# Optimization experiments

Measured on AMD Instinct MI355X. Metric: run time of the kernel, lower is better.

The kernel has to match this reference:

```python
import jax, jax.numpy as jnp
import numpy as np

B, C, H, W = 16, 256, 32, 32
AD, SC, R = 16, 32, 4


def _conv1x1(x, w, b):
    # x: [B,Cin,H,W], w: [Cout,Cin], b: [Cout]
    return jnp.einsum('oc,bchw->bohw', w, x) + b[None, :, None, None]


def setup_inputs() -> dict:
    key = jax.random.key(0)
    ks = jax.random.split(key, 12)
    p = lambda k, shape: (jax.random.normal(k, shape, dtype=jnp.float32) * 0.02)
    return {
        'x': jax.random.normal(ks[0], (B, C, H, W), dtype=jnp.float32),
        'fc1_w': p(ks[1], (C // R, C)), 'fc1_b': jnp.zeros((C // R,), jnp.float32),
        'fc2_w': p(ks[2], (C, C // R)), 'fc2_b': jnp.zeros((C,), jnp.float32),
        'qkv_w': p(ks[3], (AD * 2 + SC, SC)), 'qkv_b': jnp.zeros((AD * 2 + SC,), jnp.float32),
        'proj_w': p(ks[4], (SC, SC)), 'proj_b': jnp.zeros((SC,), jnp.float32),
        'ffn1_w': p(ks[5], (4 * C, C)), 'ffn1_b': jnp.zeros((4 * C,), jnp.float32),
        'ffn2_w': p(ks[6], (C, 4 * C)), 'ffn2_b': jnp.zeros((C,), jnp.float32),
    }


def reference(x, fc1_w, fc1_b, fc2_w, fc2_b, qkv_w, qkv_b, proj_w, proj_b,
              ffn1_w, ffn1_b, ffn2_w, ffn2_b):
    # --- DynamicChannelSelect: SE gate then channel split ---
    s = x.mean(axis=(2, 3), keepdims=True)                       # [B,C,1,1]
    s = jax.nn.relu(_conv1x1(s, fc1_w, fc1_b))
    s = jax.nn.sigmoid(_conv1x1(s, fc2_w, fc2_b))
    xg = x * s
    attn_part, non_attn_part = xg[:, :SC], xg[:, SC:]

    # --- SHSA: single-head self-attention on SC channels ---
    qkv = _conv1x1(attn_part, qkv_w, qkv_b)                      # [B,2*AD+SC,H,W]
    q = qkv[:, :AD].reshape(B, AD, H * W)
    k = qkv[:, AD:2 * AD].reshape(B, AD, H * W)
    v = qkv[:, 2 * AD:].reshape(B, SC, H * W)
    scale = AD ** -0.5
    attn = jax.nn.softmax(jnp.einsum('bcn,bcm->bnm', q, k) * scale, axis=-1)  # [B,N,N]
    out = jnp.einsum('bcm,bnm->bcn', v, attn).reshape(B, SC, H, W)
    attn_out = _conv1x1(out, proj_w, proj_b)

    # --- concat + 1x1-conv FFN ---
    y = jnp.concatenate([attn_out, non_attn_part], axis=1)       # [B,C,H,W]
    h = jax.nn.relu(_conv1x1(y, ffn1_w, ffn1_b))                 # [B,4C,H,W]
    return _conv1x1(h, ffn2_w, ffn2_b)                           # [B,C,H,W]
```

## Files before the change

### kernel.cpp

```cpp
#include <hip/hip_runtime.h>
#include <cstdint>
#include <cstddef>

#define BB 16
#define CC 256
#define NP 1024

typedef __attribute__((ext_vector_type(8))) short bf16x8;
typedef __attribute__((ext_vector_type(4))) float f32x4;
typedef unsigned short u16;

__device__ __forceinline__ u16 f2bf(float f) {
    union { float f; uint32_t u; } v; v.f = f;
    uint32_t u = v.u;
    return (u16)((u + 0x7FFFu + ((u >> 16) & 1u)) >> 16);
}

__global__ __launch_bounds__(256)
void se_mean_kernel(const float* __restrict__ x, float* __restrict__ s_mean) {
    int bc = blockIdx.x;
    const float* p = x + (size_t)bc * NP;
    int t = threadIdx.x;
    float4 v = *(const float4*)(p + t * 4);
    float s = (v.x + v.y) + (v.z + v.w);
#pragma unroll
    for (int off = 32; off; off >>= 1) s += __shfl_down(s, off, 64);
    __shared__ float red[4];
    if ((t & 63) == 0) red[t >> 6] = s;
    __syncthreads();
    if (t == 0) s_mean[bc] = (red[0] + red[1] + red[2] + red[3]) * (1.0f / NP);
}

__global__ __launch_bounds__(256)
void se_mlp_kernel(const float* __restrict__ s_mean,
                   const float* __restrict__ fc1_w, const float* __restrict__ fc1_b,
                   const float* __restrict__ fc2_w, const float* __restrict__ fc2_b,
                   float* __restrict__ sig) {
    int b = blockIdx.x;
    __shared__ float sm[CC];
    __shared__ float h1[64];
    int t = threadIdx.x;
    sm[t] = s_mean[b * CC + t];
    __syncthreads();
    if (t < 64) {
        float a = fc1_b[t];
        for (int c = 0; c < CC; ++c) a += fc1_w[t * CC + c] * sm[c];
        h1[t] = fmaxf(a, 0.f);
    }
    __syncthreads();
    float a = fc2_b[t];
#pragma unroll 8
    for (int c = 0; c < 64; ++c) a += fc2_w[t * 64 + c] * h1[c];
    sig[b * CC + t] = 1.f / (1.f + __expf(-a));
}

__global__ __launch_bounds__(256)
void scale_transpose_qkv_kernel(const float* __restrict__ x, const float* __restrict__ sig,
                                const float* __restrict__ qW, const float* __restrict__ qB,
                                u16* __restrict__ ygt, u16* __restrict__ Qt,
                                u16* __restrict__ Kt, u16* __restrict__ Vb) {
    int nt = blockIdx.x, ct = blockIdx.y, b = blockIdx.z;
    __shared__ float tile[64][65];
    __shared__ float ws[64 * 32];
    __shared__ float bs[64];
    __shared__ float vtile[32][64];
    int t = threadIdx.x;
    const float* Xb = x + ((size_t)b * CC + ct * 64) * NP + nt * 64;
    if (ct == 0) {
        for (int e = t; e < 2048; e += 256) ws[e] = qW[e];
        if (t < 64) bs[t] = qB[t];
    }
#pragma unroll
    for (int p = 0; p < 4; ++p) {
        int e = t + p * 256;
        int c = e >> 4, n4 = (e & 15) * 4;
        float4 v = *(const float4*)&Xb[(size_t)c * NP + n4];
        float sc = sig[b * CC + ct * 64 + c];
        v.x *= sc; v.y *= sc; v.z *= sc; v.w *= sc;
        tile[c][n4] = v.x; tile[c][n4 + 1] = v.y; tile[c][n4 + 2] = v.z; tile[c][n4 + 3] = v.w;
    }
    __syncthreads();
    u16* Yb = ygt + ((size_t)b * NP + nt * 64) * CC + ct * 64;
#pragma unroll
    for (int p = 0; p < 4; ++p) {
        int e = t + p * 256;
        int n = e >> 4, c4 = (e & 15) * 4;
        if (ct * 64 + c4 >= 32) {
            ushort4 o;
            o.x = f2bf(tile[c4][n]);     o.y = f2bf(tile[c4 + 1][n]);
            o.z = f2bf(tile[c4 + 2][n]); o.w = f2bf(tile[c4 + 3][n]);
            *(ushort4*)&Yb[(size_t)n * CC + c4] = o;
        }
    }
    if (ct == 0) {
        int nn = t & 63, g = t >> 6;
        int n = nt * 64 + nn;
        float acc[16];
#pragma unroll
        for (int oc = 0; oc < 16; ++oc) {
            int o = g * 16 + oc;
            float a = bs[o];
#pragma unroll
            for (int c = 0; c < 32; ++c) a += ws[o * 32 + c] * tile[c][nn];
            acc[oc] = a;
        }
        if (g == 0) {
            u16* qr = Qt + ((size_t)b * NP + n) * 32;
            ushort4 z4; z4.x = 0; z4.y = 0; z4.z = 0; z4.w = 0;
#pragma unroll
            for (int j = 0; j < 16; j += 4) {
                ushort4 o4;
                o4.x = f2bf(acc[j] * 0.25f);     o4.y = f2bf(acc[j + 1] * 0.25f);
                o4.z = f2bf(acc[j + 2] * 0.25f); o4.w = f2bf(acc[j + 3] * 0.25f);
                *(ushort4*)&qr[j] = o4;
            }
            *(ushort4*)&qr[16] = z4; *(ushort4*)&qr[20] = z4;
            *(ushort4*)&qr[24] = z4; *(ushort4*)&qr[28] = z4;
        } else if (g == 1) {
            u16* kr = Kt + ((size_t)b * NP + n) * 32;
            ushort4 z4; z4.x = 0; z4.y = 0; z4.z = 0; z4.w = 0;
#pragma unroll
            for (int j = 0; j < 16; j += 4) {
                ushort4 k4;
                k4.x = f2bf(acc[j]);     k4.y = f2bf(acc[j + 1]);
                k4.z = f2bf(acc[j + 2]); k4.w = f2bf(acc[j + 3]);
                *(ushort4*)&kr[j] = k4;
            }
            *(ushort4*)&kr[16] = z4; *(ushort4*)&kr[20] = z4;
            *(ushort4*)&kr[24] = z4; *(ushort4*)&kr[28] = z4;
        } else {
#pragma unroll
            for (int oc = 0; oc < 16; ++oc) vtile[(g - 2) * 16 + oc][nn] = acc[oc];
        }
        __syncthreads();
        for (int e = t; e < 2048; e += 256) {
            int c = e >> 6, nn2 = e & 63;
            Vb[(size_t)b * 32 * NP + (size_t)c * NP + nt * 64 + nn2] = f2bf(vtile[c][nn2]);
        }
    }
}

__global__ __launch_bounds__(512)
void attn_mfma_kernel(const u16* __restrict__ Qt, const u16* __restrict__ Kt,
                      const u16* __restrict__ Vb,
                      const float* __restrict__ proj_w, const float* __restrict__ proj_b,
                      u16* __restrict__ ygt) {
    int b = blockIdx.x >> 4;
    int n0 = (blockIdx.x & 15) * 64;
    __shared__ __align__(16) u16 P_lds[8][16][40];
    __shared__ float al_lds[8][16];
    __shared__ float sm_lds[8][16];
    __shared__ float sl_lds[8][16];
    __shared__ float O_lds[8][16][33];
    __shared__ float pw_s[32][32];
    __shared__ float pb_s[32];
    int t = threadIdx.x;
    int w = t >> 6, lane = t & 63;
    int q = lane >> 4, idx = lane & 15;
    int rg = w & 3, kh = w >> 2;

    for (int e = t; e < 1024; e += 512) pw_s[e >> 5][e & 31] = proj_w[e];
    if (t < 32) pb_s[t] = proj_b[t];
    __syncthreads();

    const u16* Qb = Qt + (size_t)b * NP * 32;
    const u16* Kb = Kt + (size_t)b * NP * 32;
    const u16* Vp = Vb + (size_t)b * 32 * NP;

    int nrow = n0 + rg * 16 + idx;
    bf16x8 aq = *(const bf16x8*)&Qb[(size_t)nrow * 32 + q * 8];

    f32x4 O0 = {0.f, 0.f, 0.f, 0.f}, O1 = {0.f, 0.f, 0.f, 0.f};
    float m_run[4] = {-1e30f, -1e30f, -1e30f, -1e30f};
    float l_run[4] = {0.f, 0.f, 0.f, 0.f};

    int mbase = kh * 512;
    for (int m0 = mbase; m0 < mbase + 512; m0 += 32) {
        bf16x8 bk0 = *(const bf16x8*)&Kb[(size_t)(m0 + idx) * 32 + q * 8];
        bf16x8 bk1 = *(const bf16x8*)&Kb[(size_t)(m0 + 16 + idx) * 32 + q * 8];
        bf16x8 va0 = *(const bf16x8*)&Vp[(size_t)idx * NP + m0 + q * 8];
        bf16x8 va1 = *(const bf16x8*)&Vp[(size_t)(16 + idx) * NP + m0 + q * 8];
        f32x4 z = {0.f, 0.f, 0.f, 0.f};
        f32x4 S0 = __builtin_amdgcn_mfma_f32_16x16x32_bf16(aq, bk0, z, 0, 0, 0);
        f32x4 S1 = __builtin_amdgcn_mfma_f32_16x16x32_bf16(aq, bk1, z, 0, 0, 0);
        float mx[4], p0[4], p1[4], alpha[4];
#pragma unroll
        for (int r = 0; r < 4; ++r) mx[r] = fmaxf(S0[r], S1[r]);
#pragma unroll
        for (int off = 1; off < 16; off <<= 1)
#pragma unroll
            for (int r = 0; r < 4; ++r) mx[r] = fmaxf(mx[r], __shfl_xor(mx[r], off, 64));
#pragma unroll
        for (int r = 0; r < 4; ++r) {
            float nm = fmaxf(m_run[r], mx[r]);
            alpha[r] = __expf(m_run[r] - nm);
            m_run[r] = nm;
            p0[r] = __expf(S0[r] - nm);
            p1[r] = __expf(S1[r] - nm);
        }
#pragma unroll
        for (int r = 0; r < 4; ++r) {
            float s = p0[r] + p1[r];
#pragma unroll
            for (int off = 1; off < 16; off <<= 1) s += __shfl_xor(s, off, 64);
            l_run[r] = l_run[r] * alpha[r] + s;
        }
#pragma unroll
        for (int r = 0; r < 4; ++r) {
            P_lds[w][q * 4 + r][idx]      = f2bf(p0[r]);
            P_lds[w][q * 4 + r][idx + 16] = f2bf(p1[r]);
        }
        if (idx == 0) {
#pragma unroll
            for (int r = 0; r < 4; ++r) al_lds[w][q * 4 + r] = alpha[r];
        }
        float an = al_lds[w][idx];
#pragma unroll
        for (int r = 0; r < 4; ++r) { O0[r] *= an; O1[r] *= an; }
        bf16x8 pf = *(const bf16x8*)&P_lds[w][idx][q * 8];
        O0 = __builtin_amdgcn_mfma_f32_16x16x32_bf16(va0, pf, O0, 0, 0, 0);
        O1 = __builtin_amdgcn_mfma_f32_16x16x32_bf16(va1, pf, O1, 0, 0, 0);
    }
    if (idx == 0) {
#pragma unroll
        for (int r = 0; r < 4; ++r) {
            sm_lds[w][q * 4 + r] = m_run[r];
            sl_lds[w][q * 4 + r] = l_run[r];
        }
    }
#pragma unroll
    for (int r = 0; r < 4; ++r) {
        O_lds[w][idx][q * 4 + r]      = O0[r];
        O_lds[w][idx][q * 4 + r + 16] = O1[r];
    }
    __syncthreads();
    if (w < 4) {
        float ma = sm_lds[w][idx], mb = sm_lds[w + 4][idx];
        float la = sl_lds[w][idx], lb = sl_lds[w + 4][idx];
        float gm = fmaxf(ma, mb);
        float ea = __expf(ma - gm), eb = __expf(mb - gm);
        float linv = 1.f / (la * ea + lb * eb);
#pragma unroll
        for (int r = 0; r < 4; ++r) {
            int c0 = q * 4 + r;
            O_lds[w][idx][c0]      = (O_lds[w][idx][c0] * ea + O_lds[w + 4][idx][c0] * eb) * linv;
            O_lds[w][idx][c0 + 16] = (O_lds[w][idx][c0 + 16] * ea + O_lds[w + 4][idx][c0 + 16] * eb) * linv;
        }
        float o0[4], o1[4];
#pragma unroll
        for (int r = 0; r < 4; ++r) { o0[r] = pb_s[q * 4 + r]; o1[r] = pb_s[q * 4 + r + 16]; }
#pragma unroll
        for (int c = 0; c < 32; ++c) {
            float xv = O_lds[w][idx][c];
#pragma unroll
            for (int r = 0; r < 4; ++r) {
                o0[r] += pw_s[q * 4 + r][c] * xv;
                o1[r] += pw_s[q * 4 + r + 16][c] * xv;
            }
        }
        u16* yrow = ygt + ((size_t)b * NP + n0 + w * 16 + idx) * CC;
        ushort4 w0, w1;
        w0.x = f2bf(o0[0]); w0.y = f2bf(o0[1]); w0.z = f2bf(o0[2]); w0.w = f2bf(o0[3]);
        w1.x = f2bf(o1[0]); w1.y = f2bf(o1[1]); w1.z = f2bf(o1[2]); w1.w = f2bf(o1[3]);
        *(ushort4*)&yrow[q * 4] = w0;
        *(ushort4*)&yrow[q * 4 + 16] = w1;
    }
}

__global__ __launch_bounds__(256)
void convert_w_kernel(const float* __restrict__ w1, u16* __restrict__ d1,
                      const float* __restrict__ w2, u16* __restrict__ d2) {
    int blk = blockIdx.x;
    const float* src = (blk < 256) ? w1 : w2;
    u16* dst = (blk < 256) ? d1 : d2;
    int i = ((blk & 255) * 256 + threadIdx.x) * 4;
    float4 v = *(const float4*)(src + i);
    ushort4 o;
    o.x = f2bf(v.x); o.y = f2bf(v.y); o.z = f2bf(v.z); o.w = f2bf(v.w);
    *(ushort4*)(dst + i) = o;
}

template <int K, bool RELU, bool TRANS_OUT>
__global__ __launch_bounds__(256)
void mfma_gemm_kernel(const u16* __restrict__ A, const u16* __restrict__ Bt,
                      const float* __restrict__ bias, void* __restrict__ Yv, int M) {
    __shared__ __align__(16) u16 As[2][128][64];
    __shared__ __align__(16) u16 Bs[2][128][64];
    constexpr int NIT = K / 64;
    int mt = blockIdx.x, nt = blockIdx.y;
    const u16* Ab = A + (size_t)mt * 128 * K;
    const u16* Bb = Bt + (size_t)nt * 128 * K;
    int t = threadIdx.x;
    int w = t >> 6, lane = t & 63;
    int q = lane >> 4, idx = lane & 15;
    int wr = (w >> 1) * 64, wc = (w & 1) * 64;
    int srow = lane >> 3;
    int gch = (lane & 7) ^ srow;

    f32x4 acc[4][4];
#pragma unroll
    for (int i = 0; i < 4; ++i)
#pragma unroll
        for (int j = 0; j < 4; ++j) { f32x4 z = {0.f, 0.f, 0.f, 0.f}; acc[i][j] = z; }

#define ISSUE_LOADS(buf, k0)                                                              \
    {                                                                                     \
        _Pragma("unroll")                                                                 \
        for (int p = 0; p < 4; ++p) {                                                     \
            int r = w * 32 + p * 8 + srow;                                                \
            __builtin_amdgcn_global_load_lds(                                             \
                (const __attribute__((address_space(1))) void*)(Ab + (size_t)r * K + (k0) + gch * 8), \
                (__attribute__((address_space(3))) void*)(&As[buf][w * 32 + p * 8][0]),   \
                16, 0, 0);                                                                \
        }                                                                                 \
        _Pragma("unroll")                                                                 \
        for (int p = 0; p < 4; ++p) {                                                     \
            int r = w * 32 + p * 8 + srow;                                                \
            __builtin_amdgcn_global_load_lds(                                             \
                (const __attribute__((address_space(1))) void*)(Bb + (size_t)r * K + (k0) + gch * 8), \
                (__attribute__((address_space(3))) void*)(&Bs[buf][w * 32 + p * 8][0]),   \
                16, 0, 0);                                                                \
        }                                                                                 \
    }

    ISSUE_LOADS(0, 0)
    for (int ki = 0; ki < NIT; ++ki) {
        int cur = ki & 1;
        __syncthreads();
        if (ki + 1 < NIT) ISSUE_LOADS(cur ^ 1, (ki + 1) * 64)
#pragma unroll
        for (int h = 0; h < 2; ++h) {
            bf16x8 af[4], bfr[4];
#pragma unroll
            for (int i = 0; i < 4; ++i)
                af[i] = *(const bf16x8*)&As[cur][wr + i * 16 + idx][(((q + 4 * h) ^ (idx & 7)) * 8)];
#pragma unroll
            for (int j = 0; j < 4; ++j)
                bfr[j] = *(const bf16x8*)&Bs[cur][wc + j * 16 + idx][(((q + 4 * h) ^ (idx & 7)) * 8)];
#pragma unroll
            for (int i = 0; i < 4; ++i)
#pragma unroll
                for (int j = 0; j < 4; ++j)
                    acc[i][j] = __builtin_amdgcn_mfma_f32_16x16x32_bf16(af[i], bfr[j], acc[i][j], 0, 0, 0);
        }
    }
#undef ISSUE_LOADS

    if (TRANS_OUT) {
        u16* Y = (u16*)Yv;
#pragma unroll
        for (int i = 0; i < 4; ++i) {
            int m0 = mt * 128 + wr + i * 16 + q * 4;
            float b0 = bias[m0], b1 = bias[m0 + 1], b2 = bias[m0 + 2], b3 = bias[m0 + 3];
#pragma unroll
            for (int j = 0; j < 4; ++j) {
                int n = nt * 128 + wc + j * 16 + idx;
                f32x4 v = acc[i][j];
                float r0 = v.x + b0, r1 = v.y + b1, r2 = v.z + b2, r3 = v.w + b3;
                if (RELU) {
                    r0 = fmaxf(r0, 0.f); r1 = fmaxf(r1, 0.f);
                    r2 = fmaxf(r2, 0.f); r3 = fmaxf(r3, 0.f);
                }
                ushort4 o;
                o.x = f2bf(r0); o.y = f2bf(r1); o.z = f2bf(r2); o.w = f2bf(r3);
                *(ushort4*)&Y[(size_t)n * (size_t)M + m0] = o;
            }
        }
    } else {
        float* Y = (float*)Yv;
#pragma unroll
        for (int i = 0; i < 4; ++i) {
            int m0 = mt * 128 + wr + i * 16 + q * 4;
            float b0 = bias[m0], b1 = bias[m0 + 1], b2 = bias[m0 + 2], b3 = bias[m0 + 3];
#pragma unroll
            for (int j = 0; j < 4; ++j) {
                int ng = nt * 128 + wc + j * 16 + idx;
                int bb = ng >> 10, nn = ng & 1023;
                f32x4 v = acc[i][j];
                float* p = Y + ((size_t)bb * M + m0) * NP + nn;
                p[0]      = v.x + b0;
                p[NP]     = v.y + b1;
                p[2 * NP] = v.z + b2;
                p[3 * NP] = v.w + b3;
            }
        }
    }
}

extern "C" void kernel_launch(void* const* d_in, const int* in_sizes, int n_in,
                              void* d_out, int out_size, void* d_ws, size_t ws_size,
                              hipStream_t stream) {
    const float* x      = (const float*)d_in[0];
    const float* fc1_w  = (const float*)d_in[1];
    const float* fc1_b  = (const float*)d_in[2];
    const float* fc2_w  = (const float*)d_in[3];
    const float* fc2_b  = (const float*)d_in[4];
    const float* qkv_w  = (const float*)d_in[5];
    const float* qkv_b  = (const float*)d_in[6];
    const float* proj_w = (const float*)d_in[7];
    const float* proj_b = (const float*)d_in[8];
    const float* ffn1_w = (const float*)d_in[9];
    const float* ffn1_b = (const float*)d_in[10];
    const float* ffn2_w = (const float*)d_in[11];
    const float* ffn2_b = (const float*)d_in[12];
    float* out = (float*)d_out;

    u16* w1b = (u16*)d_ws;
    u16* w2b = w1b + 262144;
    u16* ygt = w2b + 262144;
    u16* ht  = ygt + (size_t)BB * NP * CC;
    float* sig    = (float*)ht;
    float* s_mean = sig + BB * CC;
    u16* Qt = (u16*)(s_mean + BB * CC);
    u16* Kt = Qt + (size_t)BB * NP * 32;
    u16* Vb = Kt + (size_t)BB * NP * 32;

    se_mean_kernel<<<BB * CC, 256, 0, stream>>>(x, s_mean);
    convert_w_kernel<<<512, 256, 0, stream>>>(ffn1_w, w1b, ffn2_w, w2b);
    se_mlp_kernel<<<BB, 256, 0, stream>>>(s_mean, fc1_w, fc1_b, fc2_w, fc2_b, sig);
    scale_transpose_qkv_kernel<<<dim3(16, 4, BB), 256, 0, stream>>>(
        x, sig, qkv_w, qkv_b, ygt, Qt, Kt, Vb);
    attn_mfma_kernel<<<BB * 16, 512, 0, stream>>>(Qt, Kt, Vb, proj_w, proj_b, ygt);

    mfma_gemm_kernel<256, true, true><<<dim3(8, 128), 256, 0, stream>>>(
        w1b, ygt, ffn1_b, (void*)ht, 1024);
    mfma_gemm_kernel<1024, false, false><<<dim3(2, 128), 256, 0, stream>>>(
        w2b, ht, ffn2_b, (void*)out, 256);
}
```

Before: 181.7 us.

## Split attention into more blocks, add N64 FFN2 GEMM tile, fuse SE mean and weight conversion

The attention kernel now handles 16 query rows per block with 4 waves, each covering a quarter of the keys, instead of 64 rows with 8 waves. That gives four times as many blocks, and the partial softmax states are merged 4-way in LDS. The second FFN GEMM gets a dedicated kernel with a 128x64 tile, doubling its grid from 256 to 512 blocks so more CUs are busy. The SE mean kernel and the weight bf16 conversion are merged into one launch. The cost is more redundant K/V and proj-weight loads across blocks, and a serial 4-way merge done by a single wave.

Result: no change. 180.1 us (-0.9%).

```diff
diff --git a/kernel.cpp b/kernel.cpp
--- a/kernel.cpp
+++ b/kernel.cpp
@@ -17,18 +17,31 @@
 }
 
 __global__ __launch_bounds__(256)
-void se_mean_kernel(const float* __restrict__ x, float* __restrict__ s_mean) {
-    int bc = blockIdx.x;
-    const float* p = x + (size_t)bc * NP;
-    int t = threadIdx.x;
-    float4 v = *(const float4*)(p + t * 4);
-    float s = (v.x + v.y) + (v.z + v.w);
-#pragma unroll
-    for (int off = 32; off; off >>= 1) s += __shfl_down(s, off, 64);
-    __shared__ float red[4];
-    if ((t & 63) == 0) red[t >> 6] = s;
-    __syncthreads();
-    if (t == 0) s_mean[bc] = (red[0] + red[1] + red[2] + red[3]) * (1.0f / NP);
+void se_mean_conv_kernel(const float* __restrict__ x, float* __restrict__ s_mean,
+                         const float* __restrict__ w1, u16* __restrict__ d1,
+                         const float* __restrict__ w2, u16* __restrict__ d2) {
+    int blk = blockIdx.x;
+    int t = threadIdx.x;
+    if (blk < BB * CC) {
+        const float* p = x + (size_t)blk * NP;
+        float4 v = *(const float4*)(p + t * 4);
+        float s = (v.x + v.y) + (v.z + v.w);
+#pragma unroll
+        for (int off = 32; off; off >>= 1) s += __shfl_down(s, off, 64);
+        __shared__ float red[4];
+        if ((t & 63) == 0) red[t >> 6] = s;
+        __syncthreads();
+        if (t == 0) s_mean[blk] = (red[0] + red[1] + red[2] + red[3]) * (1.0f / NP);
+    } else {
+        int blk2 = blk - BB * CC;
+        const float* src = (blk2 < 256) ? w1 : w2;
+        u16* dst = (blk2 < 256) ? d1 : d2;
+        int i = ((blk2 & 255) * 256 + t) * 4;
+        float4 v = *(const float4*)(src + i);
+        ushort4 o;
+        o.x = f2bf(v.x); o.y = f2bf(v.y); o.z = f2bf(v.z); o.w = f2bf(v.w);
+        *(ushort4*)(dst + i) = o;
+    }
 }
 
 __global__ __launch_bounds__(256)
@@ -140,26 +153,25 @@
     }
 }
 
-__global__ __launch_bounds__(512)
+__global__ __launch_bounds__(256)
 void attn_mfma_kernel(const u16* __restrict__ Qt, const u16* __restrict__ Kt,
                       const u16* __restrict__ Vb,
                       const float* __restrict__ proj_w, const float* __restrict__ proj_b,
                       u16* __restrict__ ygt) {
-    int b = blockIdx.x >> 4;
-    int n0 = (blockIdx.x & 15) * 64;
-    __shared__ __align__(16) u16 P_lds[8][16][40];
-    __shared__ float al_lds[8][16];
-    __shared__ float sm_lds[8][16];
-    __shared__ float sl_lds[8][16];
-    __shared__ float O_lds[8][16][33];
+    int b = blockIdx.x >> 6;
+    int n0 = (blockIdx.x & 63) * 16;
+    __shared__ __align__(16) u16 P_lds[4][16][40];
+    __shared__ float al_lds[4][16];
+    __shared__ float sm_lds[4][16];
+    __shared__ float sl_lds[4][16];
+    __shared__ float O_lds[4][16][33];
     __shared__ float pw_s[32][32];
     __shared__ float pb_s[32];
     int t = threadIdx.x;
     int w = t >> 6, lane = t & 63;
     int q = lane >> 4, idx = lane & 15;
-    int rg = w & 3, kh = w >> 2;
-
-    for (int e = t; e < 1024; e += 512) pw_s[e >> 5][e & 31] = proj_w[e];
+
+    for (int e = t; e < 1024; e += 256) pw_s[e >> 5][e & 31] = proj_w[e];
     if (t < 32) pb_s[t] = proj_b[t];
     __syncthreads();
 
@@ -167,15 +179,15 @@
     const u16* Kb = Kt + (size_t)b * NP * 32;
     const u16* Vp = Vb + (size_t)b * 32 * NP;
 
-    int nrow = n0 + rg * 16 + idx;
+    int nrow = n0 + idx;
     bf16x8 aq = *(const bf16x8*)&Qb[(size_t)nrow * 32 + q * 8];
 
     f32x4 O0 = {0.f, 0.f, 0.f, 0.f}, O1 = {0.f, 0.f, 0.f, 0.f};
     float m_run[4] = {-1e30f, -1e30f, -1e30f, -1e30f};
     float l_run[4] = {0.f, 0.f, 0.f, 0.f};
 
-    int mbase = kh * 512;
-    for (int m0 = mbase; m0 < mbase + 512; m0 += 32) {
+    int mbase = w * 256;
+    for (int m0 = mbase; m0 < mbase + 256; m0 += 32) {
         bf16x8 bk0 = *(const bf16x8*)&Kb[(size_t)(m0 + idx) * 32 + q * 8];
         bf16x8 bk1 = *(const bf16x8*)&Kb[(size_t)(m0 + 16 + idx) * 32 + q * 8];
         bf16x8 va0 = *(const bf16x8*)&Vp[(size_t)idx * NP + m0 + q * 8];
@@ -234,31 +246,35 @@
         O_lds[w][idx][q * 4 + r + 16] = O1[r];
     }
     __syncthreads();
-    if (w < 4) {
-        float ma = sm_lds[w][idx], mb = sm_lds[w + 4][idx];
-        float la = sl_lds[w][idx], lb = sl_lds[w + 4][idx];
-        float gm = fmaxf(ma, mb);
-        float ea = __expf(ma - gm), eb = __expf(mb - gm);
-        float linv = 1.f / (la * ea + lb * eb);
+    if (w == 0) {
+        float m0_ = sm_lds[0][idx], m1 = sm_lds[1][idx], m2 = sm_lds[2][idx], m3 = sm_lds[3][idx];
+        float gm = fmaxf(fmaxf(m0_, m1), fmaxf(m2, m3));
+        float e0 = __expf(m0_ - gm), e1 = __expf(m1 - gm);
+        float e2 = __expf(m2 - gm), e3 = __expf(m3 - gm);
+        float linv = 1.f / (sl_lds[0][idx] * e0 + sl_lds[1][idx] * e1 +
+                            sl_lds[2][idx] * e2 + sl_lds[3][idx] * e3);
 #pragma unroll
         for (int r = 0; r < 4; ++r) {
             int c0 = q * 4 + r;
-            O_lds[w][idx][c0]      = (O_lds[w][idx][c0] * ea + O_lds[w + 4][idx][c0] * eb) * linv;
-            O_lds[w][idx][c0 + 16] = (O_lds[w][idx][c0 + 16] * ea + O_lds[w + 4][idx][c0 + 16] * eb) * linv;
+            O_lds[0][idx][c0] = (O_lds[0][idx][c0] * e0 + O_lds[1][idx][c0] * e1 +
+                                 O_lds[2][idx][c0] * e2 + O_lds[3][idx][c0] * e3) * linv;
+            int c1 = c0 + 16;
+            O_lds[0][idx][c1] = (O_lds[0][idx][c1] * e0 + O_lds[1][idx][c1] * e1 +
+                                 O_lds[2][idx][c1] * e2 + O_lds[3][idx][c1] * e3) * linv;
         }
         float o0[4], o1[4];
 #pragma unroll
         for (int r = 0; r < 4; ++r) { o0[r] = pb_s[q * 4 + r]; o1[r] = pb_s[q * 4 + r + 16]; }
 #pragma unroll
         for (int c = 0; c < 32; ++c) {
-            float xv = O_lds[w][idx][c];
+            float xv = O_lds[0][idx][c];
 #pragma unroll
             for (int r = 0; r < 4; ++r) {
                 o0[r] += pw_s[q * 4 + r][c] * xv;
                 o1[r] += pw_s[q * 4 + r + 16][c] * xv;
             }
         }
-        u16* yrow = ygt + ((size_t)b * NP + n0 + w * 16 + idx) * CC;
+        u16* yrow = ygt + ((size_t)b * NP + n0 + idx) * CC;
         ushort4 w0, w1;
         w0.x = f2bf(o0[0]); w0.y = f2bf(o0[1]); w0.z = f2bf(o0[2]); w0.w = f2bf(o0[3]);
         w1.x = f2bf(o1[0]); w1.y = f2bf(o1[1]); w1.z = f2bf(o1[2]); w1.w = f2bf(o1[3]);
@@ -267,23 +283,10 @@
     }
 }
 
-__global__ __launch_bounds__(256)
-void convert_w_kernel(const float* __restrict__ w1, u16* __restrict__ d1,
-                      const float* __restrict__ w2, u16* __restrict__ d2) {
-    int blk = blockIdx.x;
-    const float* src = (blk < 256) ? w1 : w2;
-    u16* dst = (blk < 256) ? d1 : d2;
-    int i = ((blk & 255) * 256 + threadIdx.x) * 4;
-    float4 v = *(const float4*)(src + i);
-    ushort4 o;
-    o.x = f2bf(v.x); o.y = f2bf(v.y); o.z = f2bf(v.z); o.w = f2bf(v.w);
-    *(ushort4*)(dst + i) = o;
-}
-
-template <int K, bool RELU, bool TRANS_OUT>
+template <int K, bool RELU>
 __global__ __launch_bounds__(256)
 void mfma_gemm_kernel(const u16* __restrict__ A, const u16* __restrict__ Bt,
-                      const float* __restrict__ bias, void* __restrict__ Yv, int M) {
+                      const float* __restrict__ bias, u16* __restrict__ Y, int M) {
     __shared__ __align__(16) u16 As[2][128][64];
     __shared__ __align__(16) u16 Bs[2][128][64];
     constexpr int NIT = K / 64;
@@ -346,43 +349,106 @@
     }
 #undef ISSUE_LOADS
 
-    if (TRANS_OUT) {
-        u16* Y = (u16*)Yv;
-#pragma unroll
-        for (int i = 0; i < 4; ++i) {
-            int m0 = mt * 128 + wr + i * 16 + q * 4;
-            float b0 = bias[m0], b1 = bias[m0 + 1], b2 = bias[m0 + 2], b3 = bias[m0 + 3];
-#pragma unroll
-            for (int j = 0; j < 4; ++j) {
-                int n = nt * 128 + wc + j * 16 + idx;
-                f32x4 v = acc[i][j];
-                float r0 = v.x + b0, r1 = v.y + b1, r2 = v.z + b2, r3 = v.w + b3;
-                if (RELU) {
-                    r0 = fmaxf(r0, 0.f); r1 = fmaxf(r1, 0.f);
-                    r2 = fmaxf(r2, 0.f); r3 = fmaxf(r3, 0.f);
-                }
-                ushort4 o;
-                o.x = f2bf(r0); o.y = f2bf(r1); o.z = f2bf(r2); o.w = f2bf(r3);
-                *(ushort4*)&Y[(size_t)n * (size_t)M + m0] = o;
+#pragma unroll
+    for (int i = 0; i < 4; ++i) {
+        int m0 = mt * 128 + wr + i * 16 + q * 4;
+        float b0 = bias[m0], b1 = bias[m0 + 1], b2 = bias[m0 + 2], b3 = bias[m0 + 3];
+#pragma unroll
+        for (int j = 0; j < 4; ++j) {
+            int n = nt * 128 + wc + j * 16 + idx;
+            f32x4 v = acc[i][j];
+            float r0 = v.x + b0, r1 = v.y + b1, r2 = v.z + b2, r3 = v.w + b3;
+            if (RELU) {
+                r0 = fmaxf(r0, 0.f); r1 = fmaxf(r1, 0.f);
+                r2 = fmaxf(r2, 0.f); r3 = fmaxf(r3, 0.f);
             }
-        }
-    } else {
-        float* Y = (float*)Yv;
-#pragma unroll
-        for (int i = 0; i < 4; ++i) {
-            int m0 = mt * 128 + wr + i * 16 + q * 4;
-            float b0 = bias[m0], b1 = bias[m0 + 1], b2 = bias[m0 + 2], b3 = bias[m0 + 3];
-#pragma unroll
-            for (int j = 0; j < 4; ++j) {
-                int ng = nt * 128 + wc + j * 16 + idx;
-                int bb = ng >> 10, nn = ng & 1023;
-                f32x4 v = acc[i][j];
-                float* p = Y + ((size_t)bb * M + m0) * NP + nn;
-                p[0]      = v.x + b0;
-                p[NP]     = v.y + b1;
-                p[2 * NP] = v.z + b2;
-                p[3 * NP] = v.w + b3;
-            }
+            ushort4 o;
+            o.x = f2bf(r0); o.y = f2bf(r1); o.z = f2bf(r2); o.w = f2bf(r3);
+            *(ushort4*)&Y[(size_t)n * (size_t)M + m0] = o;
+        }
+    }
+}
+
+template <int K>
+__global__ __launch_bounds__(256)
+void mfma_gemm_n64_kernel(const u16* __restrict__ A, const u16* __restrict__ Bt,
+                          const float* __restrict__ bias, float* __restrict__ Y, int M) {
+    __shared__ __align__(16) u16 As[2][128][64];
+    __shared__ __align__(16) u16 Bs[2][64][64];
+    constexpr int NIT = K / 64;
+    int mt = blockIdx.x, nt = blockIdx.y;
+    const u16* Ab = A + (size_t)mt * 128 * K;
+    const u16* Bb = Bt + (size_t)nt * 64 * K;
+    int t = threadIdx.x;
+    int w = t >> 6, lane = t & 63;
+    int q = lane >> 4, idx = lane & 15;
+    int wr = (w >> 1) * 64, wc = (w & 1) * 32;
+    int srow = lane >> 3;
+    int gch = (lane & 7) ^ srow;
+
+    f32x4 acc[4][2];
+#pragma unroll
+    for (int i = 0; i < 4; ++i)
+#pragma unroll
+        for (int j = 0; j < 2; ++j) { f32x4 z = {0.f, 0.f, 0.f, 0.f}; acc[i][j] = z; }
+
+#define ISSUE_LOADS64(buf, k0)                                                            \
+    {                                                                                     \
+        _Pragma("unroll")                                                                 \
+        for (int p = 0; p < 4; ++p) {                                                     \
+            int r = w * 32 + p * 8 + srow;                                                \
+            __builtin_amdgcn_global_load_lds(                                             \
+                (const __attribute__((address_space(1))) void*)(Ab + (size_t)r * K + (k0) + gch * 8), \
+                (__attribute__((address_space(3))) void*)(&As[buf][w * 32 + p * 8][0]),   \
+                16, 0, 0);                                                                \
+        }                                                                                 \
+        _Pragma("unroll")                                                                 \
+        for (int p = 0; p < 2; ++p) {                                                     \
+            int r = w * 16 + p * 8 + srow;                                                \
+            __builtin_amdgcn_global_load_lds(                                             \
+                (const __attribute__((address_space(1))) void*)(Bb + (size_t)r * K + (k0) + gch * 8), \
+                (__attribute__((address_space(3))) void*)(&Bs[buf][w * 16 + p * 8][0]),   \
+                16, 0, 0);                                                                \
+        }                                                                                 \
+    }
+
+    ISSUE_LOADS64(0, 0)
+    for (int ki = 0; ki < NIT; ++ki) {
+        int cur = ki & 1;
+        __syncthreads();
+        if (ki + 1 < NIT) ISSUE_LOADS64(cur ^ 1, (ki + 1) * 64)
+#pragma unroll
+        for (int h = 0; h < 2; ++h) {
+            bf16x8 af[4], bfr[2];
+#pragma unroll
+            for (int i = 0; i < 4; ++i)
+                af[i] = *(const bf16x8*)&As[cur][wr + i * 16 + idx][(((q + 4 * h) ^ (idx & 7)) * 8)];
+#pragma unroll
+            for (int j = 0; j < 2; ++j)
+                bfr[j] = *(const bf16x8*)&Bs[cur][wc + j * 16 + idx][(((q + 4 * h) ^ (idx & 7)) * 8)];
+#pragma unroll
+            for (int i = 0; i < 4; ++i)
+#pragma unroll
+                for (int j = 0; j < 2; ++j)
+                    acc[i][j] = __builtin_amdgcn_mfma_f32_16x16x32_bf16(af[i], bfr[j], acc[i][j], 0, 0, 0);
+        }
+    }
+#undef ISSUE_LOADS64
+
+#pragma unroll
+    for (int i = 0; i < 4; ++i) {
+        int m0 = mt * 128 + wr + i * 16 + q * 4;
+        float b0 = bias[m0], b1 = bias[m0 + 1], b2 = bias[m0 + 2], b3 = bias[m0 + 3];
+#pragma unroll
+        for (int j = 0; j < 2; ++j) {
+            int ng = nt * 64 + wc + j * 16 + idx;
+            int bb = ng >> 10, nn = ng & 1023;
+            f32x4 v = acc[i][j];
+            float* p = Y + ((size_t)bb * M + m0) * NP + nn;
+            p[0]      = v.x + b0;
+            p[NP]     = v.y + b1;
+            p[2 * NP] = v.z + b2;
+            p[3 * NP] = v.w + b3;
         }
     }
 }
@@ -415,15 +481,14 @@
     u16* Kt = Qt + (size_t)BB * NP * 32;
     u16* Vb = Kt + (size_t)BB * NP * 32;
 
-    se_mean_kernel<<<BB * CC, 256, 0, stream>>>(x, s_mean);
-    convert_w_kernel<<<512, 256, 0, stream>>>(ffn1_w, w1b, ffn2_w, w2b);
+    se_mean_conv_kernel<<<BB * CC + 512, 256, 0, stream>>>(x, s_mean, ffn1_w, w1b, ffn2_w, w2b);
     se_mlp_kernel<<<BB, 256, 0, stream>>>(s_mean, fc1_w, fc1_b, fc2_w, fc2_b, sig);
     scale_transpose_qkv_kernel<<<dim3(16, 4, BB), 256, 0, stream>>>(
         x, sig, qkv_w, qkv_b, ygt, Qt, Kt, Vb);
-    attn_mfma_kernel<<<BB * 16, 512, 0, stream>>>(Qt, Kt, Vb, proj_w, proj_b, ygt);
-
-    mfma_gemm_kernel<256, true, true><<<dim3(8, 128), 256, 0, stream>>>(
-        w1b, ygt, ffn1_b, (void*)ht, 1024);
-    mfma_gemm_kernel<1024, false, false><<<dim3(2, 128), 256, 0, stream>>>(
-        w2b, ht, ffn2_b, (void*)out, 256);
-}
+    attn_mfma_kernel<<<BB * 64, 256, 0, stream>>>(Qt, Kt, Vb, proj_w, proj_b, ygt);
+
+    mfma_gemm_kernel<256, true><<<dim3(8, 128), 256, 0, stream>>>(
+        w1b, ygt, ffn1_b, ht, 1024);
+    mfma_gemm_n64_kernel<1024><<<dim3(2, 256), 256, 0, stream>>>(
+        w2b, ht, ffn2_b, out, 256);
+}
```
